# Optimization experiments

Hardware: AMD Instinct MI355X
Metric: run time of the kernel (lower is better)

The kernel has to match this reference:

```python
import jax, jax.numpy as jnp
import numpy as np

FEAT = 64
OUT_DIM = 64
INV_SQRT2 = 0.7071067811865476  # Haar cA of a length-1 zero-padded signal is x/sqrt(2)


def setup_inputs() -> dict:
    key = jax.random.key(0)
    k1, k2, k3, k4, k5, k6 = jax.random.split(key, 6)
    batch, node = 4, 8192
    x = jax.random.normal(k1, (batch, node, FEAT), dtype=jnp.float32)
    adj = jax.random.uniform(k2, (node, node), dtype=jnp.float32) / node  # row-normalized-ish dense adjacency
    # per-feature Linear(wave_len=1 -> 1): weight (feat,), bias (feat,)
    nl_w = jax.random.normal(k3, (FEAT,), dtype=jnp.float32)
    nl_b = jax.random.normal(k4, (FEAT,), dtype=jnp.float32) * 0.01
    # linear_out: (out_dim, feat) weight, (out_dim,) bias
    w_out = jax.random.normal(k5, (OUT_DIM, FEAT), dtype=jnp.float32) / np.sqrt(FEAT)
    b_out = jax.random.normal(k6, (OUT_DIM,), dtype=jnp.float32) * 0.01
    return {"x": x, "adj": adj, "nl_w": nl_w, "nl_b": nl_b, "w_out": w_out, "b_out": b_out}


def reference(x, adj, nl_w, nl_b, w_out, b_out):
    # agg[b,i,f] = sum_j adj[i,j] x[b,j,f]
    agg = jnp.einsum('ij,bjf->bif', adj, x)
    # Haar DWT (J=1, zero mode) of each scalar treated as a length-1 signal -> cA = agg/sqrt(2);
    # per-feature Linear(1->1) then acts elementwise across the feature axis.
    agg_nl = agg * (INV_SQRT2 * nl_w) + nl_b  # (batch, node, feat)
    # linear_out over feature dim; dropout is identity in eval mode
    out = jnp.einsum('bnf,of->bno', agg_nl, w_out) + b_out
    return out
```

## Files before the change

kernel.cpp:

```cpp
#include <hip/hip_runtime.h>

#define NODE 8192
#define FEAT 64
#define OUTD 64
#define NCOL 256

typedef float f32x4 __attribute__((ext_vector_type(4)));
typedef short s16x8 __attribute__((ext_vector_type(8)));
typedef short s16x4 __attribute__((ext_vector_type(4)));
typedef int   i32x4 __attribute__((ext_vector_type(4)));

__device__ __forceinline__ short f2bf(float f) {
    unsigned u = __builtin_bit_cast(unsigned, f);
    u += 0x7FFFu + ((u >> 16) & 1u);
    return (short)(u >> 16);
}

__device__ __forceinline__ s16x8 pack8(const f32x4& a, const f32x4& b) {
    s16x8 r;
#pragma unroll
    for (int i = 0; i < 4; ++i) r[i] = f2bf(a[i]);
#pragma unroll
    for (int i = 0; i < 4; ++i) r[4 + i] = f2bf(b[i]);
    return r;
}

__device__ __forceinline__ void gl2lds16(const float* g, float* l) {
    __builtin_amdgcn_global_load_lds(
        (const __attribute__((address_space(1))) void*)g,
        (__attribute__((address_space(3))) void*)l, 16, 0, 0);
}

__global__ void bias2_kernel(const float* __restrict__ nl_b,
                             const float* __restrict__ w_out,
                             const float* __restrict__ b_out,
                             float* __restrict__ bias2) {
    __shared__ float part[4][64];
    const int o = threadIdx.x & 63;
    const int fc = threadIdx.x >> 6;
    float s = 0.f;
#pragma unroll
    for (int i = 0; i < 16; ++i) {
        int f = fc * 16 + i;
        s += nl_b[f] * w_out[o * FEAT + f];
    }
    part[fc][o] = s;
    __syncthreads();
    if (fc == 0)
        bias2[o] = b_out[o] + part[0][o] + part[1][o] + part[2][o] + part[3][o];
}

__global__ __launch_bounds__(256) void init_out_kernel(
    float* __restrict__ out, const float* __restrict__ bias2) {
    const int idx = (int)blockIdx.x * 256 + threadIdx.x;
    f32x4 bv = *(const f32x4*)(bias2 + ((idx & 15) << 2));
    *(f32x4*)(out + (size_t)idx * 4) = bv;
}

__global__ __launch_bounds__(256) void build_ybf_kernel(
    const float* __restrict__ x, const float* __restrict__ nl_w,
    const float* __restrict__ w_out, unsigned short* __restrict__ ybf) {
    __shared__ float xs[128 * 65];
    __shared__ float w2t[64 * 68];
    const int tid = threadIdx.x;
    const int b   = (int)blockIdx.x >> 6;
    const int j0  = ((int)blockIdx.x & 63) << 7;

    const f32x4* src = (const f32x4*)(x + ((size_t)b * NODE + j0) * FEAT);
#pragma unroll
    for (int it = 0; it < 8; ++it) {
        int i = tid + it * 256;
        f32x4 v = src[i];
        int jl = i >> 4, f0 = (i & 15) << 2;
        float* d = &xs[jl * 65 + f0];
        d[0] = v[0]; d[1] = v[1]; d[2] = v[2]; d[3] = v[3];
    }
#pragma unroll
    for (int it = 0; it < 16; ++it) {
        int i = tid + it * 256;
        int o = i >> 6, f = i & 63;
        w2t[f * 68 + o] = w_out[i] * (0.70710678118654752f * nl_w[f]);
    }
    __syncthreads();

    const int oq = tid & 15;
    const int J  = tid >> 4;
    const float* xr = &xs[(J * 8) * 65];
    const float* wr = &w2t[oq * 4];

    float acc[4][8];
#pragma unroll
    for (int i = 0; i < 4; ++i)
#pragma unroll
        for (int e = 0; e < 8; ++e) acc[i][e] = 0.f;

#pragma unroll 4
    for (int f = 0; f < 64; ++f) {
        f32x4 w4 = *(const f32x4*)(wr + f * 68);
        float xv[8];
#pragma unroll
        for (int e = 0; e < 8; ++e) xv[e] = xr[e * 65 + f];
#pragma unroll
        for (int i = 0; i < 4; ++i)
#pragma unroll
            for (int e = 0; e < 8; ++e) acc[i][e] += w4[i] * xv[e];
    }

    const int jn0 = j0 + J * 8;
    const int kb  = jn0 >> 5;
    const int q   = (jn0 >> 3) & 3;
    const int c16 = b * 4 + (oq >> 2);
    unsigned short* dst = ybf + ((size_t)(c16 * 256 + kb) * 512) +
                          q * 128 + ((oq & 3) * 4) * 8;
#pragma unroll
    for (int i = 0; i < 4; ++i) {
        s16x8 pv;
#pragma unroll
        for (int e = 0; e < 8; ++e) pv[e] = f2bf(acc[i][e]);
        *(s16x8*)(dst + i * 8) = pv;
    }
}

__global__ __launch_bounds__(256, 2) void gemm_adj_kernel(
    const float* __restrict__ adj, const unsigned short* __restrict__ ybf,
    float* __restrict__ out) {
    __shared__ __align__(16) float As[4][4][1024];

    const int tid  = threadIdx.x;
    const int lane = tid & 63;
    const int wv   = tid >> 6;
    const int bi   = (int)blockIdx.x;
    const int xcd  = bi & 7;
    const int w    = bi >> 3;
    const int cg   = w & 3;
    const int ks   = (w >> 2) & 7;
    const int rg   = (w >> 5) * 8 + xcd;
    const int row0 = rg * 128 + wv * 32;
    const int t16  = lane & 15;
    const int quad = lane >> 4;

    const float* aSrc[4];
#pragma unroll
    for (int g = 0; g < 4; ++g)
        aSrc[g] = adj + (size_t)(row0 + g * 8 + (lane >> 3)) * NODE +
                  ks * 1024 + 4 * ((lane & 7) ^ (lane >> 3));

    int aIdx[2][2];
#pragma unroll
    for (int m = 0; m < 2; ++m)
#pragma unroll
        for (int h = 0; h < 2; ++h)
            aIdx[m][h] = (m * 16 + t16) * 32 +
                         (((quad * 2 + h) ^ (lane & 7)) << 2);

    const unsigned short* bpB[4];
#pragma unroll
    for (int nt = 0; nt < 4; ++nt)
        bpB[nt] = ybf + ((size_t)((cg * 4 + nt) * 256 + ks * 32) * 512) + lane * 8;

    i32x4 BF[2][4];
    f32x4 acc[2][4];
#pragma unroll
    for (int mi = 0; mi < 2; ++mi)
#pragma unroll
        for (int nt = 0; nt < 4; ++nt) acc[mi][nt] = (f32x4){0.f, 0.f, 0.f, 0.f};

#pragma unroll
    for (int s = 0; s < 4; ++s)
#pragma unroll
        for (int g = 0; g < 4; ++g)
            gl2lds16(aSrc[g] + s * 32, &As[wv][s][g * 256]);
    __builtin_amdgcn_sched_barrier(0);
#pragma unroll
    for (int nt = 0; nt < 4; ++nt) BF[0][nt] = *(const i32x4*)bpB[nt];
#pragma unroll
    for (int nt = 0; nt < 4; ++nt) BF[1][nt] = *(const i32x4*)(bpB[nt] + 512);

#define ROUND(qv, PH, BP)                                                     \
    {                                                                         \
        asm volatile("s_waitcnt vmcnt(12)" ::: "memory");                     \
        __builtin_amdgcn_sched_barrier(0);                                    \
        const float* sb = &As[wv][PH][0];                                     \
        f32x4 a00 = *(const f32x4*)(sb + aIdx[0][0]);                         \
        f32x4 a01 = *(const f32x4*)(sb + aIdx[0][1]);                         \
        f32x4 a10 = *(const f32x4*)(sb + aIdx[1][0]);                         \
        f32x4 a11 = *(const f32x4*)(sb + aIdx[1][1]);                         \
        s16x8 af0 = pack8(a00, a01);                                          \
        s16x8 af1 = pack8(a10, a11);                                          \
        _Pragma("unroll") for (int nt = 0; nt < 4; ++nt) {                    \
            s16x8 bf = __builtin_bit_cast(s16x8, BF[BP][nt]);                 \
            acc[0][nt] = __builtin_amdgcn_mfma_f32_16x16x32_bf16(             \
                af0, bf, acc[0][nt], 0, 0, 0);                                \
            acc[1][nt] = __builtin_amdgcn_mfma_f32_16x16x32_bf16(             \
                af1, bf, acc[1][nt], 0, 0, 0);                                \
        }                                                                     \
        {                                                                     \
            const int tB = ((qv) + 2) & 31;                                   \
            _Pragma("unroll") for (int nt = 0; nt < 4; ++nt)                  \
                BF[BP][nt] = *(const i32x4*)(bpB[nt] + (size_t)tB * 512);     \
        }                                                                     \
        __builtin_amdgcn_sched_barrier(0);                                    \
        {                                                                     \
            const int tA = ((qv) + 4) & 31;                                   \
            _Pragma("unroll") for (int g = 0; g < 4; ++g)                     \
                gl2lds16(aSrc[g] + tA * 32, &As[wv][PH][g * 256]);            \
        }                                                                     \
        __builtin_amdgcn_sched_barrier(0);                                    \
    }

#pragma unroll 1
    for (int q = 0; q < 32; q += 4) {
        ROUND(q + 0, 0, 0)
        ROUND(q + 1, 1, 1)
        ROUND(q + 2, 2, 0)
        ROUND(q + 3, 3, 1)
    }
#undef ROUND

    asm volatile("s_waitcnt vmcnt(0)" ::: "memory");
    __builtin_amdgcn_sched_barrier(0);

#pragma unroll
    for (int mi = 0; mi < 2; ++mi) {
        const int i0 = row0 + mi * 16 + quad * 4;
#pragma unroll
        for (int nt = 0; nt < 4; ++nt) {
            float* op = out + ((size_t)cg * NODE + i0) * OUTD + nt * 16 + t16;
#pragma unroll
            for (int rr = 0; rr < 4; ++rr)
                atomicAdd(op + (size_t)rr * OUTD, acc[mi][nt][rr]);
        }
    }
}

extern "C" void kernel_launch(void* const* d_in, const int* in_sizes, int n_in,
                              void* d_out, int out_size, void* d_ws, size_t ws_size,
                              hipStream_t stream) {
    const float* x     = (const float*)d_in[0];
    const float* adj   = (const float*)d_in[1];
    const float* nl_w  = (const float*)d_in[2];
    const float* nl_b  = (const float*)d_in[3];
    const float* w_out = (const float*)d_in[4];
    const float* b_out = (const float*)d_in[5];
    float* out = (float*)d_out;

    unsigned short* ybf = (unsigned short*)d_ws;
    float* bias2 = (float*)((char*)d_ws + (size_t)NCOL * NODE * 2);

    bias2_kernel<<<1, 256, 0, stream>>>(nl_b, w_out, b_out, bias2);
    init_out_kernel<<<2048, 256, 0, stream>>>(out, bias2);
    build_ybf_kernel<<<256, 256, 0, stream>>>(x, nl_w, w_out, ybf);
    gemm_adj_kernel<<<2048, 256, 0, stream>>>(adj, ybf, out);
}
```

Before: 467.1 us.

## Replace split-K atomics with intra-block K reduction through LDS

Instead of splitting K across 8 blocks and accumulating partial sums into out with atomics, each block now owns 32 rows and its four waves split K into 2048-column chunks. The partial tiles are reduced in shared memory and written once with the bias added. This removes the out-initialisation kernel and the global atomic traffic. In exchange, the grid halves to 1024 blocks and each wave does twice as many K iterations, which may reduce parallelism and latency hiding.

```diff
diff --git a/kernel.cpp b/kernel.cpp
--- a/kernel.cpp
+++ b/kernel.cpp
@@ -50,13 +50,6 @@
         bias2[o] = b_out[o] + part[0][o] + part[1][o] + part[2][o] + part[3][o];
 }
 
-__global__ __launch_bounds__(256) void init_out_kernel(
-    float* __restrict__ out, const float* __restrict__ bias2) {
-    const int idx = (int)blockIdx.x * 256 + threadIdx.x;
-    f32x4 bv = *(const f32x4*)(bias2 + ((idx & 15) << 2));
-    *(f32x4*)(out + (size_t)idx * 4) = bv;
-}
-
 __global__ __launch_bounds__(256) void build_ybf_kernel(
     const float* __restrict__ x, const float* __restrict__ nl_w,
     const float* __restrict__ w_out, unsigned short* __restrict__ ybf) {
@@ -123,7 +116,7 @@
 
 __global__ __launch_bounds__(256, 2) void gemm_adj_kernel(
     const float* __restrict__ adj, const unsigned short* __restrict__ ybf,
-    float* __restrict__ out) {
+    const float* __restrict__ bias2, float* __restrict__ out) {
     __shared__ __align__(16) float As[4][4][1024];
 
     const int tid  = threadIdx.x;
@@ -133,9 +126,8 @@
     const int xcd  = bi & 7;
     const int w    = bi >> 3;
     const int cg   = w & 3;
-    const int ks   = (w >> 2) & 7;
-    const int rg   = (w >> 5) * 8 + xcd;
-    const int row0 = rg * 128 + wv * 32;
+    const int rg   = (w >> 2) * 8 + xcd;
+    const int row0 = rg * 32;
     const int t16  = lane & 15;
     const int quad = lane >> 4;
 
@@ -143,7 +135,7 @@
 #pragma unroll
     for (int g = 0; g < 4; ++g)
         aSrc[g] = adj + (size_t)(row0 + g * 8 + (lane >> 3)) * NODE +
-                  ks * 1024 + 4 * ((lane & 7) ^ (lane >> 3));
+                  wv * 2048 + 4 * ((lane & 7) ^ (lane >> 3));
 
     int aIdx[2][2];
 #pragma unroll
@@ -156,7 +148,7 @@
     const unsigned short* bpB[4];
 #pragma unroll
     for (int nt = 0; nt < 4; ++nt)
-        bpB[nt] = ybf + ((size_t)((cg * 4 + nt) * 256 + ks * 32) * 512) + lane * 8;
+        bpB[nt] = ybf + ((size_t)((cg * 4 + nt) * 256 + wv * 64) * 512) + lane * 8;
 
     i32x4 BF[2][4];
     f32x4 acc[2][4];
@@ -195,13 +187,13 @@
                 af1, bf, acc[1][nt], 0, 0, 0);                                \
         }                                                                     \
         {                                                                     \
-            const int tB = ((qv) + 2) & 31;                                   \
+            const int tB = ((qv) + 2) & 63;                                   \
             _Pragma("unroll") for (int nt = 0; nt < 4; ++nt)                  \
                 BF[BP][nt] = *(const i32x4*)(bpB[nt] + (size_t)tB * 512);     \
         }                                                                     \
         __builtin_amdgcn_sched_barrier(0);                                    \
         {                                                                     \
-            const int tA = ((qv) + 4) & 31;                                   \
+            const int tA = ((qv) + 4) & 63;                                   \
             _Pragma("unroll") for (int g = 0; g < 4; ++g)                     \
                 gl2lds16(aSrc[g] + tA * 32, &As[wv][PH][g * 256]);            \
         }                                                                     \
@@ -209,7 +201,7 @@
     }
 
 #pragma unroll 1
-    for (int q = 0; q < 32; q += 4) {
+    for (int q = 0; q < 64; q += 4) {
         ROUND(q + 0, 0, 0)
         ROUND(q + 1, 1, 1)
         ROUND(q + 2, 2, 0)
@@ -219,17 +211,33 @@
 
     asm volatile("s_waitcnt vmcnt(0)" ::: "memory");
     __builtin_amdgcn_sched_barrier(0);
-
-#pragma unroll
-    for (int mi = 0; mi < 2; ++mi) {
-        const int i0 = row0 + mi * 16 + quad * 4;
-#pragma unroll
-        for (int nt = 0; nt < 4; ++nt) {
-            float* op = out + ((size_t)cg * NODE + i0) * OUTD + nt * 16 + t16;
+    __syncthreads();
+
+    float* pl = &As[0][0][0];
+#pragma unroll
+    for (int mi = 0; mi < 2; ++mi)
+#pragma unroll
+        for (int nt = 0; nt < 4; ++nt)
 #pragma unroll
             for (int rr = 0; rr < 4; ++rr)
-                atomicAdd(op + (size_t)rr * OUTD, acc[mi][nt][rr]);
+                pl[wv * 2048 + (mi * 16 + quad * 4 + rr) * 64 + nt * 16 + t16] =
+                    acc[mi][nt][rr];
+    __syncthreads();
+
+#pragma unroll
+    for (int cc = 0; cc < 2; ++cc) {
+        const int cid = tid * 2 + cc;
+        const int row = cid >> 4;
+        const int c4  = (cid & 15) << 2;
+        f32x4 s = *(const f32x4*)(pl + row * 64 + c4);
+#pragma unroll
+        for (int w2 = 1; w2 < 4; ++w2) {
+            f32x4 p = *(const f32x4*)(pl + w2 * 2048 + row * 64 + c4);
+            s[0] += p[0]; s[1] += p[1]; s[2] += p[2]; s[3] += p[3];
         }
+        f32x4 bb = *(const f32x4*)(bias2 + c4);
+        s[0] += bb[0]; s[1] += bb[1]; s[2] += bb[2]; s[3] += bb[3];
+        *(f32x4*)(out + ((size_t)cg * NODE + row0 + row) * OUTD + c4) = s;
     }
 }
 
@@ -248,7 +256,6 @@
     float* bias2 = (float*)((char*)d_ws + (size_t)NCOL * NODE * 2);
 
     bias2_kernel<<<1, 256, 0, stream>>>(nl_b, w_out, b_out, bias2);
-    init_out_kernel<<<2048, 256, 0, stream>>>(out, bias2);
     build_ybf_kernel<<<256, 256, 0, stream>>>(x, nl_w, w_out, ybf);
-    gemm_adj_kernel<<<2048, 256, 0, stream>>>(adj, ybf, out);
-}
+    gemm_adj_kernel<<<1024, 256, 0, stream>>>(adj, ybf, bias2, out);
+}
```

Result: faster. 450.2 us (-3.6%).
